# Optimization experiments

Measured on AMD Instinct MI355X. Metric: run time of the kernel, lower is better.

Reference implementation:

```python
import jax, jax.numpy as jnp
import numpy as np

IN_DIM = 64; OUT_DIM = 128; B = 4; N = 256
GRID_SIZE = 5; ORDER = 3; NUM_BASIS = GRID_SIZE + ORDER  # 8
EPS_LN = 1e-5; EPS_BN = 1e-5; TEMP = 1.0

def make_grid():
    g = jnp.linspace(-1.0, 1.0, GRID_SIZE + 1)
    h = 2.0 / GRID_SIZE
    left = g[0] - h * jnp.arange(ORDER, 0, -1, dtype=jnp.float32)
    right = g[-1] + h * jnp.arange(1, ORDER + 1, dtype=jnp.float32)
    return jnp.concatenate([left, g, right])  # (grid_size+1+2*order,) = (12,)

def kan_layer(x, base_w, spline_w, coeffs):
    # x: (rows, in_features); eval mode (dropout = identity)
    grid = make_grid()
    x = jnp.tanh(x)
    base_out = jax.nn.silu(x) @ base_w.T
    xe = x[..., None]  # (rows, in, 1)
    bases = ((xe >= grid[:-1]) & (xe < grid[1:])).astype(x.dtype)  # (rows, in, 11)
    for k in range(1, ORDER + 1):  # Cox-de Boor recursion
        dl = jnp.clip(grid[k:-1] - grid[:-k - 1], 1e-8)
        dr = jnp.clip(grid[k + 1:] - grid[1:-k], 1e-8)
        bases = (xe - grid[:-k - 1]) / dl * bases[..., :-1] + (grid[k + 1:] - xe) / dr * bases[..., 1:]
    # bases: (rows, in, NUM_BASIS)
    sc = jnp.clip(coeffs, -5.0, 5.0) * spline_w[..., None]  # (out, in, NUM_BASIS)
    return base_out + jnp.einsum('bij,oij->bo', bases, sc)

def layer_norm(x, g, b):
    m = x.mean(-1, keepdims=True)
    v = x.var(-1, keepdims=True)
    return (x - m) * jax.lax.rsqrt(v + EPS_LN) * g + b

def setup_inputs() -> dict:
    key = jax.random.key(0)
    ks = jax.random.split(key, 12)
    def r(k, shape, s=1.0):
        return jax.random.normal(k, shape, jnp.float32) * s
    return {
        "h": r(ks[0], (B, N, IN_DIM)),
        "ln_in_g": jnp.ones((IN_DIM,), jnp.float32), "ln_in_b": jnp.zeros((IN_DIM,), jnp.float32),
        "ln_p_g": jnp.ones((IN_DIM,), jnp.float32), "ln_p_b": jnp.zeros((IN_DIM,), jnp.float32),
        "ka_bw": r(ks[1], (IN_DIM, IN_DIM), 0.05), "ka_sw": r(ks[2], (IN_DIM, IN_DIM), 0.05),
        "ka_c": r(ks[3], (IN_DIM, IN_DIM, NUM_BASIS), 0.001),
        "W_att": r(ks[4], (IN_DIM, N), 0.05),
        "kp_bw": r(ks[5], (OUT_DIM, IN_DIM), 0.05), "kp_sw": r(ks[6], (OUT_DIM, IN_DIM), 0.05),
        "kp_c": r(ks[7], (OUT_DIM, IN_DIM, NUM_BASIS), 0.001),
        "kd_bw": r(ks[8], (OUT_DIM, IN_DIM), 0.05), "kd_sw": r(ks[9], (OUT_DIM, IN_DIM), 0.05),
        "kd_c": r(ks[10], (OUT_DIM, IN_DIM, NUM_BASIS), 0.001),
        "bn_g": jnp.ones((OUT_DIM,), jnp.float32), "bn_b": jnp.zeros((OUT_DIM,), jnp.float32),
        "bn_mean": r(ks[11], (OUT_DIM,), 0.1), "bn_var": jnp.ones((OUT_DIM,), jnp.float32),
    }

def reference(h, ln_in_g, ln_in_b, ln_p_g, ln_p_b, ka_bw, ka_sw, ka_c, W_att,
              kp_bw, kp_sw, kp_c, kd_bw, kd_sw, kd_c, bn_g, bn_b, bn_mean, bn_var):
    b, n, d = h.shape
    h = layer_norm(h, ln_in_g, ln_in_b)
    hn = h / jnp.clip(jnp.linalg.norm(h, axis=-1, keepdims=True), 1e-12)
    prod = hn[:, :, None, :] * hn[:, None, :, :]          # (B, N, N, D) pairwise products
    prod = layer_norm(prod, ln_p_g, ln_p_b)
    kan_out = jnp.tanh(kan_layer(prod.reshape(-1, d), ka_bw, ka_sw, ka_c)).reshape(b, n, n, d)
    # einsum('bnmd,dk->bnmk') followed by mean over k == contraction with mean of W_att over k
    w_mean = W_att.mean(axis=1)                           # (D,)
    scores = jnp.einsum('bnmd,d->bnm', kan_out, w_mean)
    attn = jax.nn.softmax(scores / (jnp.sqrt(jnp.float32(d)) * TEMP), axis=-1)
    h_att = jnp.einsum('bnm,bmd->bnd', attn, h)
    out2 = kan_layer(h_att.reshape(-1, d), kp_bw, kp_sw, kp_c).reshape(b, n, OUT_DIM)
    out3 = kan_layer(h.reshape(-1, d), kd_bw, kd_sw, kd_c).reshape(b, n, OUT_DIM)
    out = out2 + out3
    # BatchNorm1d over channel dim, eval mode (running stats)
    out = (out - bn_mean) * jax.lax.rsqrt(bn_var + EPS_BN) * bn_g + bn_b
    return out
```

## Files before the change

kernel.cpp:

```cpp
#include <hip/hip_runtime.h>
#include <hip/hip_bf16.h>
#include <stdint.h>

#define BBATCH 4
#define NSEQ   256
#define DIN    64
#define DOUT   128
#define NBASIS 8
#define KTOT   576
#define K2TOT  1152
#define NSTEP  18
#define XST16  68

typedef __attribute__((ext_vector_type(8))) __bf16 bf16x8;
typedef __attribute__((ext_vector_type(4))) float  f32x4;

__device__ __forceinline__ float wave_sum(float v){
#pragma unroll
  for (int m = 1; m < 64; m <<= 1) v += __shfl_xor(v, m, 64);
  return v;
}

__device__ __forceinline__ float fast_tanh(float y){
  y = fminf(10.f, fmaxf(-10.f, y));
  float e = __expf(2.f * y);
  return (e - 1.f) / (e + 1.f);
}

__device__ __forceinline__ float silu_f(float x){
  return __fdividef(x, 1.f + __expf(-x));
}

__device__ __forceinline__ unsigned short f2bf(float f){
  union { float f; unsigned u; } v; v.f = f;
  unsigned r = (v.u + 0x7fffu + ((v.u >> 16) & 1u)) >> 16;
  return (unsigned short)r;
}

__device__ __forceinline__ float bf2f(unsigned short s){
  union { unsigned u; float f; } v; v.u = ((unsigned)s) << 16;
  return v.f;
}

__device__ __forceinline__ float bf2f_lo(unsigned w){
  union { unsigned u; float f; } v; v.u = w << 16;
  return v.f;
}
__device__ __forceinline__ float bf2f_hi(unsigned w){
  union { unsigned u; float f; } v; v.u = w & 0xffff0000u;
  return v.f;
}

__device__ __forceinline__ unsigned pk2(float a, float b){
  union { float f; unsigned u; } ua, ub; ua.f = a; ub.f = b;
  return __builtin_amdgcn_perm(ub.u + 0x8000u, ua.u + 0x8000u, 0x07060302);
}

__device__ __forceinline__ void spline_w(float x, int &i, float w[4]){
  float u = (x + 1.f) * 2.5f;
  int ii = (int)floorf(u);
  ii = ii < 0 ? 0 : (ii > 5 ? 5 : ii);
  float t = u - (float)ii;
  float t2 = t * t, t3 = t2 * t;
  float it = 1.f - t;
  w[0] = it * it * it * (1.f/6.f);
  w[1] = (3.f*t3 - 6.f*t2 + 4.f) * (1.f/6.f);
  w[2] = (-3.f*t3 + 3.f*t2 + 3.f*t + 1.f) * (1.f/6.f);
  w[3] = t3 * (1.f/6.f);
  i = ii;
}

__device__ __forceinline__ bf16x8 spline_pack(float x){
  float u = (x + 1.f) * 2.5f;
  int ii = (int)floorf(u);
  ii = ii < 0 ? 0 : (ii > 5 ? 5 : ii);
  float t = u - (float)ii;
  float t2 = t * t, t3 = t2 * t;
  float it = 1.f - t;
  float w0 = it * it * it * (1.f/6.f);
  float w1 = (3.f*t3 - 6.f*t2 + 4.f) * (1.f/6.f);
  float w2 = (-3.f*t3 + 3.f*t2 + 3.f*t + 1.f) * (1.f/6.f);
  float w3 = t3 * (1.f/6.f);
  unsigned long long W = ((unsigned long long)pk2(w2, w3) << 32) | (unsigned long long)pk2(w0, w1);
  int s16 = ii << 4;
  unsigned long long shl_lo = W << (s16 & 63);
  unsigned long long shr    = W >> ((64 - s16) & 63);
  unsigned long long shl_hi = W << ((s16 - 64) & 63);
  bool ge4 = ii >= 4;
  unsigned long long lo = ge4 ? 0ull : shl_lo;
  unsigned long long hi = ge4 ? shl_hi : (ii == 0 ? 0ull : shr);
  union { unsigned long long q[2]; bf16x8 v8; } r;
  r.q[0] = lo; r.q[1] = hi;
  return r.v8;
}

__global__ void k_prep_all(const float* __restrict__ h,
                           const float* __restrict__ g_in, const float* __restrict__ b_in,
                           const float* __restrict__ ka_bw, const float* __restrict__ ka_sw,
                           const float* __restrict__ ka_c,  const float* __restrict__ W_att,
                           const float* __restrict__ kp_bw, const float* __restrict__ kp_sw,
                           const float* __restrict__ kp_c,
                           const float* __restrict__ kd_bw, const float* __restrict__ kd_sw,
                           const float* __restrict__ kd_c,
                           float* __restrict__ h_ln, float* __restrict__ hn,
                           unsigned short* __restrict__ S_t, float* __restrict__ wm,
                           unsigned short* __restrict__ S2){
  int blk = blockIdx.x, tid = threadIdx.x;
  if (blk < 256){
    int row = blk*4 + (tid >> 6);
    int d   = tid & 63;
    float x = h[row*DIN + d];
    float mean = wave_sum(x) * (1.f/64.f);
    float xm = x - mean;
    float var = wave_sum(xm*xm) * (1.f/64.f);
    float hl = xm * rsqrtf(var + 1e-5f) * g_in[d] + b_in[d];
    h_ln[row*DIN + d] = hl;
    float nrm = sqrtf(wave_sum(hl*hl));
    nrm = fmaxf(nrm, 1e-12f);
    hn[row*DIN + d] = hl / nrm;
  } else if (blk < 320){
    int o = blk - 256;
    int nt = o >> 4, colr = o & 15;
    for (int k = tid; k < KTOT; k += 256){
      float v;
      if (k < 64){
        v = ka_bw[o*64 + k];
      } else {
        int km = k - 64, dd = km >> 3, j = km & 7;
        float c = ka_c[(o*64 + dd)*8 + j];
        c = fminf(5.f, fmaxf(-5.f, c));
        v = c * ka_sw[o*64 + dd];
      }
      int s = k >> 5, grp = (k >> 3) & 3, e = k & 7;
      int lane = grp*16 + colr;
      S_t[((s*4 + nt)*64 + lane)*8 + e] = f2bf(v);
    }
  } else if (blk == 320){
    if (tid < 64){
      float s = 0.f;
      for (int k = 0; k < 256; ++k) s += W_att[tid*256 + k];
      wm[tid] = s * (1.f/256.f);
    }
  } else {
    int o = blk - 321;
    for (int kk = tid; kk < K2TOT; kk += 256){
      const float* bw; const float* sw; const float* cc;
      int k = kk;
      if (kk < KTOT){ bw = kp_bw; sw = kp_sw; cc = kp_c; }
      else          { bw = kd_bw; sw = kd_sw; cc = kd_c; k = kk - KTOT; }
      float v;
      if (k < 64){
        v = bw[o*64 + k];
      } else {
        int km = k - 64, d = km >> 3, j = km & 7;
        float c = cc[(o*64 + d)*8 + j];
        c = fminf(5.f, fmaxf(-5.f, c));
        v = c * sw[o*64 + d];
      }
      S2[((kk >> 3)*128 + o)*8 + (kk & 7)] = f2bf(v);
    }
  }
}

__launch_bounds__(512, 4)
__global__ void k_scores(const float* __restrict__ hn,
                         const float* __restrict__ ln_p_g, const float* __restrict__ ln_p_b,
                         const unsigned short* __restrict__ S_t,
                         const float* __restrict__ wm,
                         float* __restrict__ scores){
  __shared__ unsigned short Xs[NSEQ * XST16];
  __shared__ float hnn_l[64], g_l[64], b_l[64];

  int idx  = blockIdx.x;
  int bb   = idx & 3;
  int n    = idx >> 2;
  int sn   = n >> 5;

  int tid  = threadIdx.x;
  int lane = tid & 63, wave = tid >> 6;
  int m0   = wave * 32;
  bool active = (wave >= sn);

  if (active){
    const float* src = hn + (bb*NSEQ + m0)*DIN;
#pragma unroll
    for (int j = 0; j < 8; ++j){
      int f4 = j*64 + lane;
      float4 v = *(const float4*)(src + f4*4);
      int r = f4 >> 4, c = (f4 & 15) * 4;
      uint2 pk = { pk2(v.x, v.y), pk2(v.z, v.w) };
      *(uint2*)(Xs + (m0 + r)*XST16 + c) = pk;
    }
  }
  if (wave == 7){
    g_l[lane]   = ln_p_g[lane];
    b_l[lane]   = ln_p_b[lane];
    hnn_l[lane] = bf2f(f2bf(hn[(bb*NSEQ + n)*DIN + lane]));
  }
  __syncthreads();

  if (active){
    int r = tid >> 1, hh = tid & 1;
    unsigned short* row = Xs + r*XST16 + hh*32;
    const float* hp = hnn_l + hh*32;
    float s1 = 0.f, s2 = 0.f;
#pragma unroll
    for (int i = 0; i < 8; ++i){
      uint2 ww = *(const uint2*)(row + i*4);
      float x0 = bf2f_lo(ww.x), x1 = bf2f_hi(ww.x), x2 = bf2f_lo(ww.y), x3 = bf2f_hi(ww.y);
      float p0 = x0*hp[i*4+0], p1 = x1*hp[i*4+1], p2 = x2*hp[i*4+2], p3 = x3*hp[i*4+3];
      s1 += (p0+p1) + (p2+p3);
      s2 = fmaf(p0,p0, fmaf(p1,p1, fmaf(p2,p2, fmaf(p3,p3, s2))));
    }
    s1 += __shfl_xor(s1, 1, 64);
    s2 += __shfl_xor(s2, 1, 64);
    float mean = s1 * (1.f/64.f);
    float var  = fmaxf(s2 * (1.f/64.f) - mean*mean, 0.f);
    float inv  = rsqrtf(var + 1e-5f);
    const float* gp = g_l + hh*32;
    const float* bp = b_l + hh*32;
#pragma unroll
    for (int i = 0; i < 8; ++i){
      uint2 ww = *(const uint2*)(row + i*4);
      float x0 = bf2f_lo(ww.x), x1 = bf2f_hi(ww.x), x2 = bf2f_lo(ww.y), x3 = bf2f_hi(ww.y);
      float t0 = fast_tanh((x0*hp[i*4+0] - mean)*inv*gp[i*4+0] + bp[i*4+0]);
      float t1 = fast_tanh((x1*hp[i*4+1] - mean)*inv*gp[i*4+1] + bp[i*4+1]);
      float t2 = fast_tanh((x2*hp[i*4+2] - mean)*inv*gp[i*4+2] + bp[i*4+2]);
      float t3 = fast_tanh((x3*hp[i*4+3] - mean)*inv*gp[i*4+3] + bp[i*4+3]);
      uint2 pk = { pk2(t0, t1), pk2(t2, t3) };
      *(uint2*)(row + i*4) = pk;
    }
  }
  __syncthreads();
  if (!active) return;

  int colr = lane & 15, grp = lane >> 4;
  const unsigned short* rowA = Xs + (m0 + colr)*XST16;
  const unsigned short* rowB = Xs + (m0 + 16 + colr)*XST16;
  const unsigned short* sfp  = S_t + lane*8;

  f32x4 acc[2][4];
#pragma unroll
  for (int a = 0; a < 2; ++a)
#pragma unroll
    for (int c = 0; c < 4; ++c){ f32x4 z = {0.f,0.f,0.f,0.f}; acc[a][c] = z; }

#pragma unroll
  for (int s = 0; s < 2; ++s){
    int kw = s*32 + grp*8;
    bf16x8 bf[4];
#pragma unroll
    for (int nt = 0; nt < 4; ++nt)
      bf[nt] = *(const bf16x8*)(sfp + (s*4 + nt)*512);
    union { unsigned u[4]; bf16x8 v8; } a0, a1;
    uint2 wa0 = *(const uint2*)(rowA + kw), wa1 = *(const uint2*)(rowA + kw + 4);
    uint2 wb0 = *(const uint2*)(rowB + kw), wb1 = *(const uint2*)(rowB + kw + 4);
    a0.u[0] = pk2(silu_f(bf2f_lo(wa0.x)), silu_f(bf2f_hi(wa0.x)));
    a0.u[1] = pk2(silu_f(bf2f_lo(wa0.y)), silu_f(bf2f_hi(wa0.y)));
    a0.u[2] = pk2(silu_f(bf2f_lo(wa1.x)), silu_f(bf2f_hi(wa1.x)));
    a0.u[3] = pk2(silu_f(bf2f_lo(wa1.y)), silu_f(bf2f_hi(wa1.y)));
    a1.u[0] = pk2(silu_f(bf2f_lo(wb0.x)), silu_f(bf2f_hi(wb0.x)));
    a1.u[1] = pk2(silu_f(bf2f_lo(wb0.y)), silu_f(bf2f_hi(wb0.y)));
    a1.u[2] = pk2(silu_f(bf2f_lo(wb1.x)), silu_f(bf2f_hi(wb1.x)));
    a1.u[3] = pk2(silu_f(bf2f_lo(wb1.y)), silu_f(bf2f_hi(wb1.y)));
#pragma unroll
    for (int nt = 0; nt < 4; ++nt){
      acc[0][nt] = __builtin_amdgcn_mfma_f32_16x16x32_bf16(a0.v8, bf[nt], acc[0][nt], 0, 0, 0);
      acc[1][nt] = __builtin_amdgcn_mfma_f32_16x16x32_bf16(a1.v8, bf[nt], acc[1][nt], 0, 0, 0);
    }
  }

#pragma unroll 4
  for (int s = 2; s < NSTEP; ++s){
    int d  = (s - 2)*4 + grp;
    bf16x8 bf[4];
#pragma unroll
    for (int nt = 0; nt < 4; ++nt)
      bf[nt] = *(const bf16x8*)(sfp + (s*4 + nt)*512);
    bf16x8 a0 = spline_pack(bf2f(rowA[d]));
    bf16x8 a1 = spline_pack(bf2f(rowB[d]));
#pragma unroll
    for (int nt = 0; nt < 4; ++nt){
      acc[0][nt] = __builtin_amdgcn_mfma_f32_16x16x32_bf16(a0, bf[nt], acc[0][nt], 0, 0, 0);
      acc[1][nt] = __builtin_amdgcn_mfma_f32_16x16x32_bf16(a1, bf[nt], acc[1][nt], 0, 0, 0);
    }
  }

  float wmv[4];
#pragma unroll
  for (int nt = 0; nt < 4; ++nt) wmv[nt] = wm[nt*16 + colr];

#pragma unroll
  for (int a = 0; a < 2; ++a){
    float sacc[4] = {0.f,0.f,0.f,0.f};
#pragma unroll
    for (int nt = 0; nt < 4; ++nt){
#pragma unroll
      for (int r = 0; r < 4; ++r)
        sacc[r] += fast_tanh(acc[a][nt][r]) * wmv[nt];
    }
#pragma unroll
    for (int off = 1; off < 16; off <<= 1){
#pragma unroll
      for (int r = 0; r < 4; ++r) sacc[r] += __shfl_xor(sacc[r], off, 64);
    }
    if (colr == 0){
      int mb   = m0 + a*16 + grp*4;
      int base = (bb*NSEQ + n)*NSEQ + mb;
      float4 v = { sacc[0], sacc[1], sacc[2], sacc[3] };
      *(float4*)&scores[base] = v;
      if (wave > sn){
        int tb = bb*NSEQ*NSEQ + n;
#pragma unroll
        for (int r = 0; r < 4; ++r)
          scores[tb + (mb + r)*NSEQ] = sacc[r];
      }
    }
  }
}

__launch_bounds__(256, 4)
__global__ void k_smf(const float* __restrict__ scores,
                      const float* __restrict__ h_ln,
                      const unsigned short* __restrict__ S2,
                      const float* __restrict__ bn_g, const float* __restrict__ bn_b,
                      const float* __restrict__ bn_mean, const float* __restrict__ bn_var,
                      float* __restrict__ out){
  __shared__ float att[2][256];
  __shared__ float redm[2][2], reds[2][2];
  __shared__ float part[2][2][64];
  __shared__ float hatt[2][64];
  __shared__ float feat[2][K2TOT];
  int row0 = blockIdx.x * 2;
  int tid = threadIdx.x, lane = tid & 63, wave = tid >> 6;
  int rw = wave >> 1;
  int qw = wave & 1;
  int row = row0 + rw;
  int t128 = (qw << 6) | lane;

  float s0 = scores[row*NSEQ + t128] * 0.125f;
  float s1 = scores[row*NSEQ + 128 + t128] * 0.125f;
  float mx = fmaxf(s0, s1);
#pragma unroll
  for (int off = 1; off < 64; off <<= 1) mx = fmaxf(mx, __shfl_xor(mx, off, 64));
  if (lane == 0) redm[rw][qw] = mx;
  __syncthreads();
  mx = fmaxf(redm[rw][0], redm[rw][1]);
  float e0 = __expf(s0 - mx), e1 = __expf(s1 - mx);
  float es = wave_sum(e0 + e1);
  if (lane == 0) reds[rw][qw] = es;
  __syncthreads();
  float tot = reds[rw][0] + reds[rw][1];
  att[rw][t128]       = e0 / tot;
  att[rw][128 + t128] = e1 / tot;
  __syncthreads();

  int hb = row & ~255;
  float a2 = 0.f;
  for (int m = qw*128; m < qw*128 + 128; ++m)
    a2 += att[rw][m] * h_ln[(hb + m)*DIN + lane];
  part[rw][qw][lane] = a2;
  __syncthreads();
  if (qw == 0)
    hatt[rw][lane] = part[rw][0][lane] + part[rw][1][lane];
  __syncthreads();

  {
    int src = t128 >> 6, dd = t128 & 63;
    float x = src ? h_ln[row*DIN + dd] : hatt[rw][dd];
    x = fast_tanh(x);
    int base = src * KTOT;
    feat[rw][base + dd] = silu_f(x);
    int fb = base + 64 + dd*8;
#pragma unroll
    for (int jj = 0; jj < 8; ++jj) feat[rw][fb + jj] = 0.f;
    int i; float wgt[4];
    spline_w(x, i, wgt);
#pragma unroll
    for (int k = 0; k < 4; ++k){
      int jj = i + k;
      if (jj < 8) feat[rw][fb + jj] = wgt[k];
    }
  }
  __syncthreads();

  int o = t128;
  const unsigned short* sp = S2 + o*8;
  const float* fp = feat[rw];
  float acc = 0.f;
#pragma unroll 4
  for (int jj = 0; jj < K2TOT/8; ++jj){
    uint4  w  = *(const uint4*)(sp + jj*1024);
    float4 f0 = *(const float4*)(fp + jj*8);
    float4 f1 = *(const float4*)(fp + jj*8 + 4);
    acc = fmaf(f0.x, bf2f_lo(w.x), acc);
    acc = fmaf(f0.y, bf2f_hi(w.x), acc);
    acc = fmaf(f0.z, bf2f_lo(w.y), acc);
    acc = fmaf(f0.w, bf2f_hi(w.y), acc);
    acc = fmaf(f1.x, bf2f_lo(w.z), acc);
    acc = fmaf(f1.y, bf2f_hi(w.z), acc);
    acc = fmaf(f1.z, bf2f_lo(w.w), acc);
    acc = fmaf(f1.w, bf2f_hi(w.w), acc);
  }
  float r = (acc - bn_mean[o]) * rsqrtf(bn_var[o] + 1e-5f) * bn_g[o] + bn_b[o];
  out[row*DOUT + o] = r;
}

extern "C" void kernel_launch(void* const* d_in, const int* in_sizes, int n_in,
                              void* d_out, int out_size, void* d_ws, size_t ws_size,
                              hipStream_t stream){
  (void)in_sizes; (void)n_in; (void)out_size; (void)ws_size;
  const float* h       = (const float*)d_in[0];
  const float* ln_in_g = (const float*)d_in[1];
  const float* ln_in_b = (const float*)d_in[2];
  const float* ln_p_g  = (const float*)d_in[3];
  const float* ln_p_b  = (const float*)d_in[4];
  const float* ka_bw   = (const float*)d_in[5];
  const float* ka_sw   = (const float*)d_in[6];
  const float* ka_c    = (const float*)d_in[7];
  const float* W_att   = (const float*)d_in[8];
  const float* kp_bw   = (const float*)d_in[9];
  const float* kp_sw   = (const float*)d_in[10];
  const float* kp_c    = (const float*)d_in[11];
  const float* kd_bw   = (const float*)d_in[12];
  const float* kd_sw   = (const float*)d_in[13];
  const float* kd_c    = (const float*)d_in[14];
  const float* bn_g    = (const float*)d_in[15];
  const float* bn_b    = (const float*)d_in[16];
  const float* bn_mean = (const float*)d_in[17];
  const float* bn_var  = (const float*)d_in[18];
  float* out = (float*)d_out;

  char* ws = (char*)d_ws;
  float*          h_ln   = (float*)(ws + 0);
  float*          hn     = (float*)(ws + 262144);
  unsigned short* S_t    = (unsigned short*)(ws + 524288);
  float*          wm     = (float*)(ws + 598016);
  float*          scores = (float*)(ws + 598272);
  unsigned short* S2     = (unsigned short*)(ws + 1908992);

  k_prep_all<<<449, 256, 0, stream>>>(h, ln_in_g, ln_in_b, ka_bw, ka_sw, ka_c, W_att,
                                      kp_bw, kp_sw, kp_c, kd_bw, kd_sw, kd_c,
                                      h_ln, hn, S_t, wm, S2);
  k_scores<<<1024, 512, 0, stream>>>(hn, ln_p_g, ln_p_b, S_t, wm, scores);
  k_smf<<<512, 256, 0, stream>>>(scores, h_ln, S2, bn_g, bn_b, bn_mean, bn_var, out);
}
```

Baseline: 77.93 us.

## Pack triangular score work into dense per-wave job list

The scores kernel previously launched one block per (batch, row n) with 8 waves, idling waves below the diagonal, so about half the waves did no work. A job table of (n, column-tile) pairs covering only the upper triangle is now built in the prep kernel. Each wave of a 576-block grid takes one job and works independently on its own slice of shared memory, with no block barriers. The cost is an extra table load per wave and each wave now reloading its own hn row.

```diff
diff --git a/kernel.cpp b/kernel.cpp
--- a/kernel.cpp
+++ b/kernel.cpp
@@ -11,6 +11,7 @@
 #define K2TOT  1152
 #define NSTEP  18
 #define XST16  68
+#define NJOBS  1152
 
 typedef __attribute__((ext_vector_type(8))) __bf16 bf16x8;
 typedef __attribute__((ext_vector_type(4))) float  f32x4;
@@ -104,7 +105,8 @@
                            const float* __restrict__ kd_c,
                            float* __restrict__ h_ln, float* __restrict__ hn,
                            unsigned short* __restrict__ S_t, float* __restrict__ wm,
-                           unsigned short* __restrict__ S2){
+                           unsigned short* __restrict__ S2,
+                           unsigned short* __restrict__ jobs){
   int blk = blockIdx.x, tid = threadIdx.x;
   if (blk < 256){
     int row = blk*4 + (tid >> 6);
@@ -141,6 +143,15 @@
       for (int k = 0; k < 256; ++k) s += W_att[tid*256 + k];
       wm[tid] = s * (1.f/256.f);
     }
+    const int offs[9] = {0,256,480,672,832,960,1056,1120,1152};
+    for (int f = tid; f < NJOBS; f += 256){
+      int t = 0;
+      while (f >= offs[t+1]) ++t;
+      int r = f - offs[t];
+      int n = t*32 + r / (8 - t);
+      int w = t + r % (8 - t);
+      jobs[f] = (unsigned short)((n << 3) | w);
+    }
   } else {
     int o = blk - 321;
     for (int kk = tid; kk < K2TOT; kk += 256){
@@ -167,42 +178,45 @@
                          const float* __restrict__ ln_p_g, const float* __restrict__ ln_p_b,
                          const unsigned short* __restrict__ S_t,
                          const float* __restrict__ wm,
+                         const unsigned short* __restrict__ jobs,
                          float* __restrict__ scores){
   __shared__ unsigned short Xs[NSEQ * XST16];
-  __shared__ float hnn_l[64], g_l[64], b_l[64];
-
-  int idx  = blockIdx.x;
-  int bb   = idx & 3;
-  int n    = idx >> 2;
-  int sn   = n >> 5;
+  __shared__ float hnn_l[8][64];
+  __shared__ float g_l[64], b_l[64];
+
+  int blkid = blockIdx.x;
+  int bb    = blkid / 144;
+  int jb    = (blkid % 144) * 8;
 
   int tid  = threadIdx.x;
   int lane = tid & 63, wave = tid >> 6;
-  int m0   = wave * 32;
-  bool active = (wave >= sn);
-
-  if (active){
-    const float* src = hn + (bb*NSEQ + m0)*DIN;
+  int job  = jobs[jb + wave];
+  int n    = job >> 3;
+  int w    = job & 7;
+  int sn   = n >> 5;
+  int m0g  = w * 32;
+  int lr0  = wave * 32;
+
+  g_l[lane] = ln_p_g[lane];
+  b_l[lane] = ln_p_b[lane];
+  hnn_l[wave][lane] = bf2f(f2bf(hn[(bb*NSEQ + n)*DIN + lane]));
+
+  {
+    const float* src = hn + (bb*NSEQ + m0g)*DIN;
 #pragma unroll
     for (int j = 0; j < 8; ++j){
       int f4 = j*64 + lane;
       float4 v = *(const float4*)(src + f4*4);
       int r = f4 >> 4, c = (f4 & 15) * 4;
       uint2 pk = { pk2(v.x, v.y), pk2(v.z, v.w) };
-      *(uint2*)(Xs + (m0 + r)*XST16 + c) = pk;
-    }
-  }
-  if (wave == 7){
-    g_l[lane]   = ln_p_g[lane];
-    b_l[lane]   = ln_p_b[lane];
-    hnn_l[lane] = bf2f(f2bf(hn[(bb*NSEQ + n)*DIN + lane]));
-  }
-  __syncthreads();
-
-  if (active){
-    int r = tid >> 1, hh = tid & 1;
-    unsigned short* row = Xs + r*XST16 + hh*32;
-    const float* hp = hnn_l + hh*32;
+      *(uint2*)(Xs + (lr0 + r)*XST16 + c) = pk;
+    }
+  }
+
+  {
+    int r = lane >> 1, hh = lane & 1;
+    unsigned short* row = Xs + (lr0 + r)*XST16 + hh*32;
+    const float* hp = hnn_l[wave] + hh*32;
     float s1 = 0.f, s2 = 0.f;
 #pragma unroll
     for (int i = 0; i < 8; ++i){
@@ -231,12 +245,10 @@
       *(uint2*)(row + i*4) = pk;
     }
   }
-  __syncthreads();
-  if (!active) return;
 
   int colr = lane & 15, grp = lane >> 4;
-  const unsigned short* rowA = Xs + (m0 + colr)*XST16;
-  const unsigned short* rowB = Xs + (m0 + 16 + colr)*XST16;
+  const unsigned short* rowA = Xs + (lr0 + colr)*XST16;
+  const unsigned short* rowB = Xs + (lr0 + 16 + colr)*XST16;
   const unsigned short* sfp  = S_t + lane*8;
 
   f32x4 acc[2][4];
@@ -305,11 +317,11 @@
       for (int r = 0; r < 4; ++r) sacc[r] += __shfl_xor(sacc[r], off, 64);
     }
     if (colr == 0){
-      int mb   = m0 + a*16 + grp*4;
+      int mb   = m0g + a*16 + grp*4;
       int base = (bb*NSEQ + n)*NSEQ + mb;
       float4 v = { sacc[0], sacc[1], sacc[2], sacc[3] };
       *(float4*)&scores[base] = v;
-      if (wave > sn){
+      if (w > sn){
         int tb = bb*NSEQ*NSEQ + n;
 #pragma unroll
         for (int r = 0; r < 4; ++r)
@@ -437,11 +449,12 @@
   unsigned short* S_t    = (unsigned short*)(ws + 524288);
   float*          wm     = (float*)(ws + 598016);
   float*          scores = (float*)(ws + 598272);
+  unsigned short* jobs   = (unsigned short*)(ws + 1646848);
   unsigned short* S2     = (unsigned short*)(ws + 1908992);
 
   k_prep_all<<<449, 256, 0, stream>>>(h, ln_in_g, ln_in_b, ka_bw, ka_sw, ka_c, W_att,
                                       kp_bw, kp_sw, kp_c, kd_bw, kd_sw, kd_c,
-                                      h_ln, hn, S_t, wm, S2);
-  k_scores<<<1024, 512, 0, stream>>>(hn, ln_p_g, ln_p_b, S_t, wm, scores);
+                                      h_ln, hn, S_t, wm, S2, jobs);
+  k_scores<<<576, 512, 0, stream>>>(hn, ln_p_g, ln_p_b, S_t, wm, jobs, scores);
   k_smf<<<512, 256, 0, stream>>>(scores, h_ln, S2, bn_g, bn_b, bn_mean, bn_var, out);
 }
```

Result: no change. 76.63 us (-1.7%).
